# Optimization experiments

Measured on AMD Instinct MI355X. Metric: run time of the kernel, lower is better.

Reference implementation:

```python
import jax, jax.numpy as jnp
import numpy as np
from jax import lax

HEADS = 8
DIM_HEAD = 64
LANDMARKS = 256
PINV_ITERS = 6
KERNEL = 33


def moore_penrose_iter_pinv(x, iters=PINV_ITERS):
    # x: [b, h, m, m]
    abs_x = jnp.abs(x)
    col = abs_x.sum(axis=-1)
    row = abs_x.sum(axis=-2)
    z = jnp.swapaxes(x, -1, -2) / (jnp.max(col) * jnp.max(row) + 1e-12)
    I = jnp.eye(x.shape[-1], dtype=x.dtype)  # broadcasts over b, h
    for _ in range(iters):
        xz = x @ z
        z = 0.25 * z @ (13.0 * I - xz @ (15.0 * I - xz @ (7.0 * I - xz)))
    return z


def setup_inputs() -> dict:
    key = jax.random.key(0)
    k1, k2, k3, k4, k5 = jax.random.split(key, 5)
    b, n, dim = 4, 8192, 512
    inner = HEADS * DIM_HEAD
    x = jax.random.normal(k1, (b, n, dim), dtype=jnp.float32)
    Wqkv = jax.random.normal(k2, (dim, inner * 3), dtype=jnp.float32) * (dim ** -0.5)
    Wout = jax.random.normal(k3, (inner, dim), dtype=jnp.float32) * (inner ** -0.5)
    bout = jax.random.normal(k4, (dim,), dtype=jnp.float32) * 0.02
    conv_w = jax.random.normal(k5, (HEADS, 1, KERNEL, 1), dtype=jnp.float32) * (KERNEL ** -0.5)
    return {"x": x, "Wqkv": Wqkv, "Wout": Wout, "bout": bout, "conv_w": conv_w}


def reference(x, Wqkv, Wout, bout, conv_w):
    b, n, dim = x.shape
    h, d, m = HEADS, DIM_HEAD, LANDMARKS
    scale = d ** -0.5
    # n is a multiple of m, so no left-padding branch; mask is None.
    qkv = x @ Wqkv  # [b, n, 3*h*d]
    q, k, v = jnp.split(qkv, 3, axis=-1)
    tohead = lambda t: t.reshape(b, n, h, d).transpose(0, 2, 1, 3)  # [b,h,n,d]
    q, k, v = tohead(q), tohead(k), tohead(v)
    q = q * scale
    l = n // m  # tokens per landmark group
    qL = q.reshape(b, h, m, l, d).sum(axis=3) / l  # [b,h,m,d]
    kL = k.reshape(b, h, m, l, d).sum(axis=3) / l
    attn1 = jax.nn.softmax(jnp.einsum('bhid,bhjd->bhij', q, kL), axis=-1)   # [b,h,n,m]
    attn2 = jax.nn.softmax(jnp.einsum('bhid,bhjd->bhij', qL, kL), axis=-1)  # [b,h,m,m]
    attn3 = jax.nn.softmax(jnp.einsum('bhid,bhjd->bhij', qL, k), axis=-1)   # [b,h,m,n]
    attn2_pinv = moore_penrose_iter_pinv(attn2, PINV_ITERS)
    out = attn1 @ (attn2_pinv @ (attn3 @ v))  # [b,h,n,d]
    # depthwise residual conv over v viewed as NCHW (C=heads, H=n, W=d)
    pad = KERNEL // 2
    res = lax.conv_general_dilated(
        v, conv_w, window_strides=(1, 1), padding=((pad, pad), (0, 0)),
        dimension_numbers=('NCHW', 'OIHW', 'NCHW'), feature_group_count=h)
    out = out + res
    out = out.transpose(0, 2, 1, 3).reshape(b, n, h * d)
    out = out @ Wout + bout
    return out
```

## Files before the change

kernel.cpp:

```cpp
#include <hip/hip_runtime.h>
#include <hip/hip_bf16.h>
#include <math.h>

#define BB 4
#define NH 8
#define NN 8192
#define DD 64
#define MM 256
#define LG 32
#define DIM 512
#define K3 1536
#define KER 33

typedef __hip_bfloat16 bf16;
typedef __attribute__((ext_vector_type(8))) short bf16x8;
typedef __attribute__((ext_vector_type(4))) float f32x4;

__device__ __forceinline__ float b2f(bf16 x) { return __bfloat162float(x); }
__device__ __forceinline__ bf16 f2b(float x) { return __float2bfloat16(x); }
__device__ __forceinline__ short f2bs(float x) { bf16 h = __float2bfloat16(x); return *reinterpret_cast<short*>(&h); }
__device__ __forceinline__ float bsf(short s) { return __uint_as_float(((unsigned int)(unsigned short)s) << 16); }
__device__ __forceinline__ float blo(unsigned int u) { return __uint_as_float(u << 16); }
__device__ __forceinline__ float bhi(unsigned int u) { return __uint_as_float(u & 0xffff0000u); }

__device__ __forceinline__ void g2lds16(const void* g, void* l) {
    __builtin_amdgcn_global_load_lds(
        (const __attribute__((address_space(1))) unsigned int*)g,
        (__attribute__((address_space(3))) unsigned int*)l, 16, 0, 0);
}

__global__ void zero_out(float* __restrict__ o) {
    o[(size_t)blockIdx.x * 256 + threadIdx.x] = 0.f;
}

__global__ void split_x(const float* __restrict__ x, short* __restrict__ xh,
                        short* __restrict__ xl) {
    size_t i = ((size_t)blockIdx.x * 256 + threadIdx.x) * 8;
    const float4* xp = (const float4*)(x + i);
    float4 v0 = xp[0], v1 = xp[1];
    float vv[8] = {v0.x, v0.y, v0.z, v0.w, v1.x, v1.y, v1.z, v1.w};
    short hb[8], lb[8];
#pragma unroll
    for (int u = 0; u < 8; u++) {
        bf16 h = f2b(vv[u]);
        hb[u] = *(short*)&h;
        lb[u] = f2bs(vv[u] - b2f(h));
    }
    *(uint4*)(xh + i) = *(uint4*)hb;
    *(uint4*)(xl + i) = *(uint4*)lb;
}

__global__ void split_wT(const float* __restrict__ W, short* __restrict__ wh,
                         short* __restrict__ wl, int Nn) {
    int idx = blockIdx.x * 256 + threadIdx.x;
    int k = idx & 511, n = idx >> 9;
    float v = W[(size_t)k * Nn + n];
    bf16 h = f2b(v);
    wh[idx] = *(short*)&h;
    wl[idx] = f2bs(v - b2f(h));
}

__global__ __launch_bounds__(256) void gemm_qkv_mfma(
        const short* __restrict__ xh, const short* __restrict__ xl,
        const short* __restrict__ wh, const short* __restrict__ wl,
        bf16* __restrict__ q, bf16* __restrict__ k, bf16* __restrict__ v) {
    __shared__ short Ah[128 * 32];
    __shared__ short Al[128 * 32];
    __shared__ short Bh[128 * 32];
    __shared__ short Bl[128 * 32];
    int orig = blockIdx.x;
    int wg = (orig & 7) * 384 + (orig >> 3);
    int by = wg / 12, bx = wg - by * 12;
    int rowBase = by * 128, colBase = bx * 128;
    int tid = threadIdx.x;
    int rl = tid >> 2;
    int ch = (tid & 3) * 8;
    int wave = tid >> 6, lane = tid & 63;
    int ln = lane & 15, quad = lane >> 4;
    int wr = (wave >> 1) * 64, wc = (wave & 1) * 64;
    f32x4 acc[4][4];
#pragma unroll
    for (int mt = 0; mt < 4; mt++)
#pragma unroll
        for (int nt = 0; nt < 4; nt++) acc[mt][nt] = (f32x4){0.f, 0.f, 0.f, 0.f};

    for (int k0 = 0; k0 < DIM; k0 += 32) {
        __syncthreads();
#pragma unroll
        for (int p = 0; p < 2; p++) {
            int r = p * 64 + rl;
            size_t ga = (size_t)(rowBase + r) * DIM + k0 + ch;
            size_t gb = (size_t)(colBase + r) * DIM + k0 + ch;
            int lo = r * 32 + ch;
            g2lds16(xh + ga, &Ah[lo]);
            g2lds16(xl + ga, &Al[lo]);
            g2lds16(wh + gb, &Bh[lo]);
            g2lds16(wl + gb, &Bl[lo]);
        }
        __syncthreads();
        bf16x8 a_h[4], a_l[4], b_h[4], b_l[4];
#pragma unroll
        for (int mt = 0; mt < 4; mt++) {
            int o = (wr + mt * 16 + ln) * 32 + quad * 8;
            a_h[mt] = *(const bf16x8*)&Ah[o];
            a_l[mt] = *(const bf16x8*)&Al[o];
        }
#pragma unroll
        for (int nt = 0; nt < 4; nt++) {
            int o = (wc + nt * 16 + ln) * 32 + quad * 8;
            b_h[nt] = *(const bf16x8*)&Bh[o];
            b_l[nt] = *(const bf16x8*)&Bl[o];
        }
#pragma unroll
        for (int mt = 0; mt < 4; mt++)
#pragma unroll
            for (int nt = 0; nt < 4; nt++) {
                acc[mt][nt] = __builtin_amdgcn_mfma_f32_16x16x32_bf16(a_h[mt], b_h[nt], acc[mt][nt], 0, 0, 0);
                acc[mt][nt] = __builtin_amdgcn_mfma_f32_16x16x32_bf16(a_l[mt], b_h[nt], acc[mt][nt], 0, 0, 0);
                acc[mt][nt] = __builtin_amdgcn_mfma_f32_16x16x32_bf16(a_h[mt], b_l[nt], acc[mt][nt], 0, 0, 0);
            }
    }
    int part = colBase >> 9;
    bf16* dst = part == 0 ? q : (part == 1 ? k : v);
    float scale = part == 0 ? 0.125f : 1.0f;
#pragma unroll
    for (int mt = 0; mt < 4; mt++)
#pragma unroll
        for (int nt = 0; nt < 4; nt++)
#pragma unroll
            for (int r = 0; r < 4; r++) {
                int row = rowBase + wr + mt * 16 + quad * 4 + r;
                int col = colBase + wc + nt * 16 + ln;
                int h = (col & 511) >> 6, d = col & 63;
                int b_ = row >> 13, n_ = row & 8191;
                size_t di = ((size_t)(b_ * NH + h) * NN + n_) * DD + d;
                dst[di] = f2b(acc[mt][nt][r] * scale);
            }
}

__global__ __launch_bounds__(256) void gemm_out_mfma(
        const bf16* __restrict__ A, const short* __restrict__ wh,
        const short* __restrict__ wl, const float* __restrict__ bias,
        float* __restrict__ C) {
    __shared__ short As[128 * 32];
    __shared__ short Bh[128 * 32];
    __shared__ short Bl[128 * 32];
    int orig = blockIdx.x;
    int wg = (orig & 7) * 128 + (orig >> 3);
    int by = wg >> 2, bx = wg & 3;
    int rowBase = by * 128, colBase = bx * 128;
    int tid = threadIdx.x;
    int rl = tid >> 2, ch = (tid & 3) * 8;
    int wave = tid >> 6, lane = tid & 63;
    int ln = lane & 15, quad = lane >> 4;
    int wr = (wave >> 1) * 64, wc = (wave & 1) * 64;
    const short* Ab = (const short*)A;
    f32x4 acc[4][4];
#pragma unroll
    for (int mt = 0; mt < 4; mt++)
#pragma unroll
        for (int nt = 0; nt < 4; nt++) acc[mt][nt] = (f32x4){0.f, 0.f, 0.f, 0.f};

    for (int k0 = 0; k0 < DIM; k0 += 32) {
        __syncthreads();
#pragma unroll
        for (int p = 0; p < 2; p++) {
            int r = p * 64 + rl;
            size_t ga = (size_t)(rowBase + r) * DIM + k0 + ch;
            size_t gb = (size_t)(colBase + r) * DIM + k0 + ch;
            int lo = r * 32 + ch;
            g2lds16(Ab + ga, &As[lo]);
            g2lds16(wh + gb, &Bh[lo]);
            g2lds16(wl + gb, &Bl[lo]);
        }
        __syncthreads();
        bf16x8 a[4], b_h[4], b_l[4];
#pragma unroll
        for (int mt = 0; mt < 4; mt++)
            a[mt] = *(const bf16x8*)&As[(wr + mt * 16 + ln) * 32 + quad * 8];
#pragma unroll
        for (int nt = 0; nt < 4; nt++) {
            int o = (wc + nt * 16 + ln) * 32 + quad * 8;
            b_h[nt] = *(const bf16x8*)&Bh[o];
            b_l[nt] = *(const bf16x8*)&Bl[o];
        }
#pragma unroll
        for (int mt = 0; mt < 4; mt++)
#pragma unroll
            for (int nt = 0; nt < 4; nt++) {
                acc[mt][nt] = __builtin_amdgcn_mfma_f32_16x16x32_bf16(a[mt], b_h[nt], acc[mt][nt], 0, 0, 0);
                acc[mt][nt] = __builtin_amdgcn_mfma_f32_16x16x32_bf16(a[mt], b_l[nt], acc[mt][nt], 0, 0, 0);
            }
    }
#pragma unroll
    for (int mt = 0; mt < 4; mt++)
#pragma unroll
        for (int nt = 0; nt < 4; nt++)
#pragma unroll
            for (int r = 0; r < 4; r++) {
                int row = rowBase + wr + mt * 16 + quad * 4 + r;
                int col = colBase + wc + nt * 16 + ln;
                C[(size_t)row * DIM + col] = acc[mt][nt][r] + bias[col];
            }
}

__global__ __launch_bounds__(256) void bgemm_pair(
        const short* __restrict__ Ah, const short* __restrict__ Al,
        const short* __restrict__ Bh, const short* __restrict__ Bl,
        short* __restrict__ oAh, short* __restrict__ oAl,
        short* __restrict__ oBh, short* __restrict__ oBl,
        float* __restrict__ oF, float scale, float alpha, int flags) {
    __shared__ short sAh[64 * 32];
    __shared__ short sAl[64 * 32];
    __shared__ short sBh[64 * 32];
    __shared__ short sBl[64 * 32];
    int bat = blockIdx.z;
    int rowBase = blockIdx.y * 64;
    int colBase = blockIdx.x * 64;
    const size_t MB = (size_t)bat * (MM * MM);
    int tid = threadIdx.x;
    int rl = tid >> 2, ch = (tid & 3) * 8;
    int wave = tid >> 6, lane = tid & 63;
    int ln = lane & 15, quad = lane >> 4;
    int wr = (wave >> 1) * 32, wc = (wave & 1) * 32;
    f32x4 acc[2][2];
#pragma unroll
    for (int mt = 0; mt < 2; mt++)
#pragma unroll
        for (int nt = 0; nt < 2; nt++) acc[mt][nt] = (f32x4){0.f, 0.f, 0.f, 0.f};

    for (int k0 = 0; k0 < MM; k0 += 32) {
        __syncthreads();
        {
            size_t ga = MB + (size_t)(rowBase + rl) * MM + k0 + ch;
            size_t gb = MB + (size_t)(colBase + rl) * MM + k0 + ch;
            int lo = rl * 32 + ch;
            g2lds16(Ah + ga, &sAh[lo]);
            g2lds16(Al + ga, &sAl[lo]);
            g2lds16(Bh + gb, &sBh[lo]);
            g2lds16(Bl + gb, &sBl[lo]);
        }
        __syncthreads();
        bf16x8 a_h[2], a_l[2], b_h[2], b_l[2];
#pragma unroll
        for (int mt = 0; mt < 2; mt++) {
            int o = (wr + mt * 16 + ln) * 32 + quad * 8;
            a_h[mt] = *(const bf16x8*)&sAh[o];
            a_l[mt] = *(const bf16x8*)&sAl[o];
        }
#pragma unroll
        for (int nt = 0; nt < 2; nt++) {
            int o = (wc + nt * 16 + ln) * 32 + quad * 8;
            b_h[nt] = *(const bf16x8*)&sBh[o];
            b_l[nt] = *(const bf16x8*)&sBl[o];
        }
#pragma unroll
        for (int mt = 0; mt < 2; mt++)
#pragma unroll
            for (int nt = 0; nt < 2; nt++) {
                acc[mt][nt] = __builtin_amdgcn_mfma_f32_16x16x32_bf16(a_h[mt], b_h[nt], acc[mt][nt], 0, 0, 0);
                acc[mt][nt] = __builtin_amdgcn_mfma_f32_16x16x32_bf16(a_l[mt], b_h[nt], acc[mt][nt], 0, 0, 0);
                acc[mt][nt] = __builtin_amdgcn_mfma_f32_16x16x32_bf16(a_h[mt], b_l[nt], acc[mt][nt], 0, 0, 0);
            }
    }
#pragma unroll
    for (int mt = 0; mt < 2; mt++)
#pragma unroll
        for (int nt = 0; nt < 2; nt++) {
            short bh4[4], bl4[4];
            int col = colBase + wc + nt * 16 + ln;
            int row0 = rowBase + wr + mt * 16 + quad * 4;
#pragma unroll
            for (int r = 0; r < 4; r++) {
                int row = row0 + r;
                float val = scale * acc[mt][nt][r];
                if (row == col) val += alpha;
                if (flags & 4) oF[MB + (size_t)row * MM + col] = val;
                short vh = f2bs(val);
                short vl = f2bs(val - bsf(vh));
                if (flags & 1) {
                    oAh[MB + (size_t)row * MM + col] = vh;
                    oAl[MB + (size_t)row * MM + col] = vl;
                }
                bh4[r] = vh; bl4[r] = vl;
            }
            if (flags & 2) {
                size_t o = MB + (size_t)col * MM + row0;
                *(uint2*)&oBh[o] = *(uint2*)bh4;
                *(uint2*)&oBl[o] = *(uint2*)bl4;
            }
        }
}

__global__ void eye7_pair(const short* __restrict__ ATh, const short* __restrict__ ATl,
                          short* __restrict__ BTh, short* __restrict__ BTl) {
    size_t base = ((size_t)blockIdx.x * 256 + threadIdx.x) * 8;
    int i0 = (int)(base & 255);
    int j = (int)((base >> 8) & 255);
    uint4 hv = *(const uint4*)&ATh[base];
    uint4 lv = *(const uint4*)&ATl[base];
    unsigned int hu[4] = {hv.x, hv.y, hv.z, hv.w};
    unsigned int lu[4] = {lv.x, lv.y, lv.z, lv.w};
    short ho[8], lo_[8];
#pragma unroll
    for (int u = 0; u < 8; u++) {
        float a = (u & 1 ? bhi(hu[u >> 1]) : blo(hu[u >> 1])) +
                  (u & 1 ? bhi(lu[u >> 1]) : blo(lu[u >> 1]));
        float v = ((i0 + u) == j ? 7.0f : 0.0f) - a;
        short vh = f2bs(v);
        ho[u] = vh;
        lo_[u] = f2bs(v - bsf(vh));
    }
    *(uint4*)&BTh[base] = *(uint4*)ho;
    *(uint4*)&BTl[base] = *(uint4*)lo_;
}

__global__ void z_init_pair(const float* __restrict__ x2, const float* __restrict__ scal,
                            short* __restrict__ zAh, short* __restrict__ zAl,
                            short* __restrict__ zBh, short* __restrict__ zBl) {
    size_t base = ((size_t)blockIdx.x * 256 + threadIdx.x) * 8;
    float inv = 1.0f / (scal[0] * scal[1] + 1e-12f);
    int c0 = (int)(base & 255);
    int r = (int)((base >> 8) & 255);
    size_t MB = (base >> 16) << 16;
    const float4* xp = (const float4*)(x2 + base);
    float4 v0 = xp[0], v1 = xp[1];
    float vv[8] = {v0.x, v0.y, v0.z, v0.w, v1.x, v1.y, v1.z, v1.w};
    short ho[8], lo_[8];
#pragma unroll
    for (int u = 0; u < 8; u++) {
        float v = vv[u] * inv;
        short vh = f2bs(v);
        ho[u] = vh; lo_[u] = f2bs(v - bsf(vh));
    }
    *(uint4*)&zBh[base] = *(uint4*)ho;
    *(uint4*)&zBl[base] = *(uint4*)lo_;
#pragma unroll
    for (int u = 0; u < 8; u++) {
        float v = x2[MB + (size_t)(c0 + u) * MM + r] * inv;
        short vh = f2bs(v);
        ho[u] = vh; lo_[u] = f2bs(v - bsf(vh));
    }
    *(uint4*)&zAh[base] = *(uint4*)ho;
    *(uint4*)&zAl[base] = *(uint4*)lo_;
}

__global__ void bgemm_t2t(const float* __restrict__ A, const float* __restrict__ B,
                          short* __restrict__ T) {
    __shared__ float As[16][64];
    __shared__ float Bs[16][64];
    int bat = blockIdx.z;
    const float* Ab = A + (size_t)bat * MM * MM;
    const float* Bb = B + (size_t)bat * MM * DD;
    short* Tb = T + (size_t)bat * DD * MM;
    int tid = threadIdx.x;
    int rowBase = blockIdx.y * 64;
    int ty = tid >> 4, tx = tid & 15;
    float acc[4][4] = {};
    for (int k0 = 0; k0 < MM; k0 += 16) {
        for (int idx = tid; idx < 64 * 16; idx += 256) {
            int r = idx >> 4, c = idx & 15;
            As[c][r] = Ab[(size_t)(rowBase + r) * MM + k0 + c];
        }
        for (int idx = tid; idx < 16 * 64; idx += 256) {
            int r = idx >> 6, c = idx & 63;
            Bs[r][c] = Bb[(size_t)(k0 + r) * DD + c];
        }
        __syncthreads();
#pragma unroll
        for (int kk = 0; kk < 16; kk++) {
            float a[4], b[4];
#pragma unroll
            for (int i = 0; i < 4; i++) a[i] = As[kk][ty * 4 + i];
#pragma unroll
            for (int j = 0; j < 4; j++) b[j] = Bs[kk][tx * 4 + j];
#pragma unroll
            for (int i = 0; i < 4; i++)
#pragma unroll
                for (int j = 0; j < 4; j++) acc[i][j] += a[i] * b[j];
        }
        __syncthreads();
    }
#pragma unroll
    for (int i = 0; i < 4; i++) {
        int r = rowBase + ty * 4 + i;
#pragma unroll
        for (int j = 0; j < 4; j++) {
            int c = tx * 4 + j;
            Tb[(size_t)c * MM + r] = f2bs(acc[i][j]);
        }
    }
}

__global__ void landmark_means(const bf16* __restrict__ q, const bf16* __restrict__ k,
                               float* __restrict__ qL, float* __restrict__ kL) {
    int idx = blockIdx.x * 256 + threadIdx.x;
    int d = idx & 63;
    int mi = (idx >> 6) & 255;
    int bh = idx >> 14;
    const bf16* qp = q + ((size_t)bh * NN + mi * LG) * DD + d;
    const bf16* kp = k + ((size_t)bh * NN + mi * LG) * DD + d;
    float sq = 0.f, sk = 0.f;
#pragma unroll
    for (int j = 0; j < LG; j++) { sq += b2f(qp[(size_t)j * DD]); sk += b2f(kp[(size_t)j * DD]); }
    qL[idx] = sq * (1.f / LG);
    kL[idx] = sk * (1.f / LG);
}

__global__ void kl_to_bf16(const float* __restrict__ kL, short* __restrict__ kl16) {
    size_t i = ((size_t)blockIdx.x * 256 + threadIdx.x) * 4;
    float4 v = *(const float4*)(kL + i);
    short o[4] = {f2bs(v.x), f2bs(v.y), f2bs(v.z), f2bs(v.w)};
    *(uint2*)&kl16[i] = *(uint2*)o;
}

__global__ void attn2_softmax(const float* __restrict__ qL, const float* __restrict__ kL,
                              float* __restrict__ x2) {
    __shared__ float qs[64];
    __shared__ float red[256];
    int bh = blockIdx.x >> 8, i = blockIdx.x & 255;
    int t = threadIdx.x;
    if (t < 64) qs[t] = qL[((size_t)bh * MM + i) * DD + t];
    __syncthreads();
    const float4* kp = (const float4*)(kL + ((size_t)bh * MM + t) * DD);
    float l = 0.f;
#pragma unroll
    for (int u = 0; u < 16; u++) {
        float4 kv = kp[u];
        l += qs[u*4+0]*kv.x + qs[u*4+1]*kv.y + qs[u*4+2]*kv.z + qs[u*4+3]*kv.w;
    }
    red[t] = l; __syncthreads();
    for (int s = 128; s > 0; s >>= 1) { if (t < s) red[t] = fmaxf(red[t], red[t + s]); __syncthreads(); }
    float mx = red[0]; __syncthreads();
    float e = __expf(l - mx);
    red[t] = e; __syncthreads();
    for (int s = 128; s > 0; s >>= 1) { if (t < s) red[t] += red[t + s]; __syncthreads(); }
    x2[((size_t)bh * MM + i) * MM + t] = e / red[0];
}

__global__ void init_scal(float* scal) {
    if (threadIdx.x == 0) { scal[0] = 0.f; scal[1] = 0.f; }
}

__global__ void rsum_max(const float* __restrict__ x2, float* scal) {
    __shared__ float red[256];
    int t = threadIdx.x;
    float v = fabsf(x2[(size_t)blockIdx.x * MM + t]);
    red[t] = v; __syncthreads();
    for (int s = 128; s > 0; s >>= 1) { if (t < s) red[t] += red[t + s]; __syncthreads(); }
    if (t == 0) atomicMax((unsigned int*)&scal[0], __float_as_uint(red[0]));
}

__global__ void csum_max(const float* __restrict__ x2, float* scal) {
    __shared__ float red[256];
    int t = threadIdx.x;
    const float* xp = x2 + (size_t)blockIdx.x * MM * MM;
    float s = 0.f;
    for (int i = 0; i < MM; i++) s += fabsf(xp[(size_t)i * MM + t]);
    red[t] = s; __syncthreads();
    for (int st = 128; st > 0; st >>= 1) { if (t < st) red[t] = fmaxf(red[t], red[t + st]); __syncthreads(); }
    if (t == 0) atomicMax((unsigned int*)&scal[1], __float_as_uint(red[0]));
}

__global__ void transpose_v(const bf16* __restrict__ v, bf16* __restrict__ vT) {
    int gw = blockIdx.x * 4 + (threadIdx.x >> 6);
    int lane = threadIdx.x & 63;
    int bh = gw >> 8;
    int c  = gw & 255;
    const bf16* vb = v + ((size_t)bh * NN + c * 32) * DD + lane;
    unsigned short buf[32];
#pragma unroll
    for (int i = 0; i < 32; i++) buf[i] = *(const unsigned short*)(vb + (size_t)i * DD);
    bf16* dst = vT + ((size_t)bh * DD + lane) * NN + c * 32;
#pragma unroll
    for (int u = 0; u < 4; u++)
        *(uint4*)(dst + u * 8) = *(uint4*)&buf[u * 8];
}

#define NJ 128
#define KS2 72
#define VS2 136
#define PS2 136
__global__ __launch_bounds__(128, 2) void attn3v_mfma(
        const float* __restrict__ qL, const bf16* __restrict__ k,
        const bf16* __restrict__ vT, float* __restrict__ t1) {
    __shared__ short ks[NJ * KS2];
    __shared__ short vs[DD * VS2];
    __shared__ short ps[2][16 * PS2];
    int g = blockIdx.x;
    int c = g & 7, t = g >> 3;
    int bh = c + 8 * (t >> 3);
    int r0 = (t & 7) * 32;
    int tid = threadIdx.x;
    int wave = tid >> 6, lane = tid & 63;
    int ln = lane & 15, quad = lane >> 4;
    int m = r0 + wave * 16 + ln;
    const float* qrow = qL + ((size_t)bh * MM + m) * DD;
    bf16x8 a0, a1;
#pragma unroll
    for (int u = 0; u < 8; u++) {
        ((short*)&a0)[u] = f2bs(qrow[quad * 8 + u]);
        ((short*)&a1)[u] = f2bs(qrow[32 + quad * 8 + u]);
    }
    const uint4* kg = (const uint4*)(k + (size_t)bh * NN * DD);
    const uint4* vg = (const uint4*)(vT + (size_t)bh * DD * NN);
    float mrow[4], lrow[4];
    f32x4 o[4];
#pragma unroll
    for (int r = 0; r < 4; r++) { mrow[r] = -1e30f; lrow[r] = 0.f; }
#pragma unroll
    for (int ct = 0; ct < 4; ct++) o[ct] = (f32x4){0.f, 0.f, 0.f, 0.f};
    short* pw = &ps[wave][0];

    for (int j0 = 0; j0 < NN; j0 += NJ) {
        __syncthreads();
#pragma unroll
        for (int it = 0; it < 8; it++) {
            int idx = it * 128 + tid;
            int row = idx >> 3, c8 = idx & 7;
            uint4 pk = kg[(size_t)(j0 + row) * 8 + c8];
            *(uint4*)&ks[row * KS2 + c8 * 8] = pk;
        }
#pragma unroll
        for (int it = 0; it < 8; it++) {
            int idx = it * 128 + tid;
            int row = idx >> 4, c8 = idx & 15;
            uint4 pv = vg[(size_t)row * (NN / 8) + (j0 / 8) + c8];
            *(uint4*)&vs[row * VS2 + c8 * 8] = pv;
        }
        __syncthreads();
        f32x4 s[8];
#pragma unroll
        for (int ct = 0; ct < 8; ct++) {
            const short* kp = &ks[(ct * 16 + ln) * KS2 + quad * 8];
            bf16x8 b0 = *(const bf16x8*)kp;
            bf16x8 b1 = *(const bf16x8*)(kp + 32);
            f32x4 cc = {0.f, 0.f, 0.f, 0.f};
            cc = __builtin_amdgcn_mfma_f32_16x16x32_bf16(a0, b0, cc, 0, 0, 0);
            cc = __builtin_amdgcn_mfma_f32_16x16x32_bf16(a1, b1, cc, 0, 0, 0);
            s[ct] = cc;
        }
#pragma unroll
        for (int r = 0; r < 4; r++) {
            float v = -1e30f;
#pragma unroll
            for (int ct = 0; ct < 8; ct++) v = fmaxf(v, s[ct][r]);
            v = fmaxf(v, __shfl_xor(v, 1));
            v = fmaxf(v, __shfl_xor(v, 2));
            v = fmaxf(v, __shfl_xor(v, 4));
            v = fmaxf(v, __shfl_xor(v, 8));
            float mn = fmaxf(mrow[r], v);
            float alpha = __expf(mrow[r] - mn);
            mrow[r] = mn;
            float psum = 0.f;
#pragma unroll
            for (int ct = 0; ct < 8; ct++) { float e = __expf(s[ct][r] - mn); s[ct][r] = e; psum += e; }
            lrow[r] = lrow[r] * alpha + psum;
#pragma unroll
            for (int c2 = 0; c2 < 4; c2++) o[c2][r] *= alpha;
        }
#pragma unroll
        for (int ct = 0; ct < 8; ct++)
#pragma unroll
            for (int r = 0; r < 4; r++)
                pw[(quad * 4 + r) * PS2 + ct * 16 + ln] = f2bs(s[ct][r]);
#pragma unroll
        for (int kstep = 0; kstep < 4; kstep++) {
            bf16x8 pa = *(const bf16x8*)&pw[ln * PS2 + kstep * 32 + quad * 8];
#pragma unroll
            for (int ct = 0; ct < 4; ct++) {
                bf16x8 pb = *(const bf16x8*)&vs[(ct * 16 + ln) * VS2 + kstep * 32 + quad * 8];
                o[ct] = __builtin_amdgcn_mfma_f32_16x16x32_bf16(pa, pb, o[ct], 0, 0, 0);
            }
        }
    }
#pragma unroll
    for (int r = 0; r < 4; r++) {
        float l = lrow[r];
        l += __shfl_xor(l, 1);
        l += __shfl_xor(l, 2);
        l += __shfl_xor(l, 4);
        l += __shfl_xor(l, 8);
        lrow[r] = 1.0f / l;
    }
#pragma unroll
    for (int ct = 0; ct < 4; ct++)
#pragma unroll
        for (int r = 0; r < 4; r++) {
            int row = r0 + wave * 16 + quad * 4 + r;
            t1[((size_t)bh * MM + row) * DD + ct * 16 + ln] = o[ct][r] * lrow[r];
        }
}

#define KLS 72
#define T2S 264
__global__ __launch_bounds__(256, 1) void attn1_mfma(
        const bf16* __restrict__ q, const short* __restrict__ kl16,
        const short* __restrict__ t2t, bf16* __restrict__ oh) {
    __shared__ short kls[MM * KLS];
    __shared__ short t2s[DD * T2S];
    __shared__ short ps1[4][16 * T2S];
    int bh = blockIdx.y;
    int n0 = blockIdx.x * 64;
    int tid = threadIdx.x;
    const short* kLb = kl16 + (size_t)bh * MM * DD;
    for (int idx = tid; idx < MM * DD / 8; idx += 256) {
        int l = idx >> 3, d8 = (idx & 7) * 8;
        *(uint4*)&kls[l * KLS + d8] = *(const uint4*)&kLb[idx * 8];
    }
    const short* t2b = t2t + (size_t)bh * DD * MM;
    for (int idx = tid; idx < DD * MM / 8; idx += 256) {
        int c = idx >> 5, r = (idx & 31) * 8;
        *(uint4*)&t2s[c * T2S + r] = *(const uint4*)&t2b[idx * 8];
    }
    __syncthreads();
    int wave = tid >> 6, lane = tid & 63;
    int ln = lane & 15, quad = lane >> 4;
    int m = n0 + wave * 16 + ln;
    const bf16* qrow = q + ((size_t)bh * NN + m) * DD;
    bf16x8 a0 = *(const bf16x8*)(qrow + quad * 8);
    bf16x8 a1 = *(const bf16x8*)(qrow + 32 + quad * 8);
    f32x4 acc[16];
#pragma unroll
    for (int nt = 0; nt < 16; nt++) {
        const short* kp = &kls[(nt * 16 + ln) * KLS + quad * 8];
        bf16x8 b0 = *(const bf16x8*)kp;
        bf16x8 b1 = *(const bf16x8*)(kp + 32);
        f32x4 c = {0.f, 0.f, 0.f, 0.f};
        c = __builtin_amdgcn_mfma_f32_16x16x32_bf16(a0, b0, c, 0, 0, 0);
        c = __builtin_amdgcn_mfma_f32_16x16x32_bf16(a1, b1, c, 0, 0, 0);
        acc[nt] = c;
    }
    float inv[4];
#pragma unroll
    for (int r = 0; r < 4; r++) {
        float v = -1e30f;
#pragma unroll
        for (int nt = 0; nt < 16; nt++) v = fmaxf(v, acc[nt][r]);
        v = fmaxf(v, __shfl_xor(v, 1));
        v = fmaxf(v, __shfl_xor(v, 2));
        v = fmaxf(v, __shfl_xor(v, 4));
        v = fmaxf(v, __shfl_xor(v, 8));
        float s = 0.f;
#pragma unroll
        for (int nt = 0; nt < 16; nt++) { float e = __expf(acc[nt][r] - v); acc[nt][r] = e; s += e; }
        s += __shfl_xor(s, 1);
        s += __shfl_xor(s, 2);
        s += __shfl_xor(s, 4);
        s += __shfl_xor(s, 8);
        inv[r] = 1.0f / s;
    }
    short* pw = &ps1[wave][0];
#pragma unroll
    for (int nt = 0; nt < 16; nt++)
#pragma unroll
        for (int r = 0; r < 4; r++)
            pw[(quad * 4 + r) * T2S + nt * 16 + ln] = f2bs(acc[nt][r]);
    __syncthreads();
    f32x4 o[4];
#pragma unroll
    for (int nt = 0; nt < 4; nt++) o[nt] = (f32x4){0.f, 0.f, 0.f, 0.f};
#pragma unroll
    for (int ks = 0; ks < 8; ks++) {
        bf16x8 pa = *(const bf16x8*)&pw[ln * T2S + ks * 32 + quad * 8];
#pragma unroll
        for (int nt = 0; nt < 4; nt++) {
            bf16x8 pb = *(const bf16x8*)&t2s[(nt * 16 + ln) * T2S + ks * 32 + quad * 8];
            o[nt] = __builtin_amdgcn_mfma_f32_16x16x32_bf16(pa, pb, o[nt], 0, 0, 0);
        }
    }
    int b_ = bh >> 3, h = bh & 7;
#pragma unroll
    for (int nt = 0; nt < 4; nt++)
#pragma unroll
        for (int r = 0; r < 4; r++) {
            int row = n0 + wave * 16 + quad * 4 + r;
            int col = nt * 16 + ln;
            oh[((size_t)(b_ * NN + row)) * DIM + h * 64 + col] = f2b(o[nt][r] * inv[r]);
        }
}

__global__ __launch_bounds__(256) void conv_add2(const bf16* __restrict__ v,
                                                 const float* __restrict__ w,
                                                 bf16* __restrict__ oh) {
    int tid = threadIdx.x;
    int c = tid & 7;
    int nsub = tid >> 3;
    int bh = blockIdx.x >> 8;
    int n = ((blockIdx.x & 255) << 5) + nsub;
    int b_ = bh >> 3, h = bh & 7;
    const bf16* vb = v + (size_t)bh * NN * DD + c * 8;
    float acc[8] = {};
#pragma unroll
    for (int t = 0; t < KER; t++) {
        int src = n + t - 16;
        if (src >= 0 && src < NN) {
            uint4 pk = *(const uint4*)(vb + (size_t)src * DD);
            float wt = w[h * KER + t];
            unsigned int ua[4] = {pk.x, pk.y, pk.z, pk.w};
#pragma unroll
            for (int j = 0; j < 4; j++) {
                acc[2 * j]     += wt * blo(ua[j]);
                acc[2 * j + 1] += wt * bhi(ua[j]);
            }
        }
    }
    size_t oidx = ((size_t)(b_ * NN + n)) * DIM + h * 64 + c * 8;
    uint4 cur = *(uint4*)&oh[oidx];
    unsigned int cu[4] = {cur.x, cur.y, cur.z, cur.w};
    short outp[8];
#pragma unroll
    for (int j = 0; j < 4; j++) {
        outp[2 * j]     = f2bs(blo(cu[j]) + acc[2 * j]);
        outp[2 * j + 1] = f2bs(bhi(cu[j]) + acc[2 * j + 1]);
    }
    *(uint4*)&oh[oidx] = *(uint4*)outp;
}


extern "C" void kernel_launch(void* const* d_in, const int* in_sizes, int n_in,
                              void* d_out, int out_size, void* d_ws, size_t ws_size,
                              hipStream_t stream) {
    const float* x    = (const float*)d_in[0];
    const float* Wqkv = (const float*)d_in[1];
    const float* Wout = (const float*)d_in[2];
    const float* bout = (const float*)d_in[3];
    const float* cw   = (const float*)d_in[4];
    float* out = (float*)d_out;

    const size_t SZ_QKV = (size_t)BB * NH * NN * DD;
    const size_t SZ_L   = (size_t)BB * NH * MM * DD;
    const size_t SZ_M2  = (size_t)BB * NH * MM * MM;

    char* p = (char*)d_ws;
    bf16* q    = (bf16*)p;  p += SZ_QKV * 2;
    bf16* v    = (bf16*)p;  p += SZ_QKV * 2;
    float* x2   = (float*)p; p += SZ_M2 * 4;
    float* zf   = (float*)p; p += SZ_M2 * 4;
    float* z2r  = (float*)p; p += SZ_M2 * 4;
    float* bAr  = (float*)p; p += SZ_M2 * 4;
    float* bBr  = (float*)p; p += SZ_M2 * 4;
    float* qL   = (float*)p; p += SZ_L * 4;
    float* kL   = (float*)p; p += SZ_L * 4;
    float* t1   = (float*)p; p += SZ_L * 4;
    short* t2t  = (short*)p; p += SZ_L * 4;
    float* scal = (float*)p; p += 2 * 4;
    size_t need = (size_t)(p - (char*)d_ws);
    bf16* k  = (bf16*)d_out;
    bf16* vT = (bf16*)d_out + SZ_QKV;
    bf16* oh = (bf16*)x2;

    short* xh  = (short*)x2;
    short* xl  = (short*)vT;
    short* wqh = (short*)bBr;
    short* wql = (short*)bBr + (size_t)K3 * DIM;
    short* woh = (short*)q;
    short* wol = (short*)q + (size_t)DIM * DIM;
    short* kl16 = (short*)t1;

    const size_t U = SZ_M2;
    short* db = (short*)d_out;
    short* bufBTh = db + 0 * U;  short* bufBTl = db + 1 * U;
    short* z2BTh  = db + 2 * U;  short* z2BTl  = db + 3 * U;
    short* zPair[2][4] = {
        { db + 4 * U, db + 5 * U, db + 6 * U, db + 7 * U },
        { db + 8 * U, db + 9 * U, db + 10 * U, db + 11 * U } };
    short* x2Ah = (short*)z2r;   short* x2Al = (short*)z2r + U;
    short* bufAh = (short*)bAr;  short* bufAl = (short*)bAr + U;
    short* bufATh = (short*)bBr; short* bufATl = (short*)bBr + U;

    if (ws_size < need) {
        zero_out<<<out_size / 256, 256, 0, stream>>>(out);
        return;
    }

    split_x<<<(int)(SZ_QKV / (256 * 8)), 256, 0, stream>>>(x, xh, xl);
    split_wT<<<(K3 * DIM) / 256, 256, 0, stream>>>(Wqkv, wqh, wql, K3);
    gemm_qkv_mfma<<<3072, 256, 0, stream>>>(xh, xl, wqh, wql, q, k, v);
    transpose_v<<<(BB * NH * MM) / 4, 256, 0, stream>>>(v, vT);
    landmark_means<<<(BB * NH * MM * DD) / 256, 256, 0, stream>>>(q, k, qL, kL);
    attn2_softmax<<<BB * NH * MM, 256, 0, stream>>>(qL, kL, x2);
    attn3v_mfma<<<256, 128, 0, stream>>>(qL, k, vT, t1);
    init_scal<<<1, 64, 0, stream>>>(scal);
    rsum_max<<<BB * NH * MM, 256, 0, stream>>>(x2, scal);
    csum_max<<<BB * NH, 256, 0, stream>>>(x2, scal);
    z_init_pair<<<(int)(SZ_M2 / (256 * 8)), 256, 0, stream>>>(
        x2, scal, zPair[0][0], zPair[0][1], zPair[0][2], zPair[0][3]);
    split_x<<<(int)(SZ_M2 / (256 * 8)), 256, 0, stream>>>(x2, x2Ah, x2Al);
    int cur = 0;
    for (int it = 0; it < 6; it++) {
        int nxt = cur ^ 1;
        bgemm_pair<<<dim3(4, 4, BB * NH), 256, 0, stream>>>(
            x2Ah, x2Al, zPair[cur][2], zPair[cur][3],
            bufAh, bufAl, bufATh, bufATl, nullptr, 1.f, 0.f, 1 | 2);
        eye7_pair<<<(int)(SZ_M2 / (256 * 8)), 256, 0, stream>>>(
            bufATh, bufATl, bufBTh, bufBTl);
        bgemm_pair<<<dim3(4, 4, BB * NH), 256, 0, stream>>>(
            bufAh, bufAl, bufBTh, bufBTl,
            nullptr, nullptr, z2BTh, z2BTl, nullptr, -1.f, 15.f, 2);
        bgemm_pair<<<dim3(4, 4, BB * NH), 256, 0, stream>>>(
            bufAh, bufAl, z2BTh, z2BTl,
            nullptr, nullptr, bufBTh, bufBTl, nullptr, -1.f, 13.f, 2);
        int fl = (it == 5) ? 4 : (1 | 2);
        bgemm_pair<<<dim3(4, 4, BB * NH), 256, 0, stream>>>(
            zPair[cur][0], zPair[cur][1], bufBTh, bufBTl,
            zPair[nxt][0], zPair[nxt][1], zPair[nxt][2], zPair[nxt][3],
            zf, 0.25f, 0.f, fl);
        cur = nxt;
    }
    bgemm_t2t<<<dim3(1, 4, BB * NH), 256, 0, stream>>>(zf, t1, t2t);
    kl_to_bf16<<<(int)(SZ_L / (256 * 4)), 256, 0, stream>>>(kL, kl16);
    attn1_mfma<<<dim3(NN / 64, BB * NH), 256, 0, stream>>>(q, kl16, t2t, oh);
    conv_add2<<<BB * NH * 256, 256, 0, stream>>>(v, cw, oh);
    split_wT<<<(DIM * DIM) / 256, 256, 0, stream>>>(Wout, woh, wol, DIM);
    gemm_out_mfma<<<1024, 256, 0, stream>>>(oh, woh, wol, bout, out);

    (void)in_sizes; (void)n_in; (void)ws_size;
}
```

Measured before the change: 1.181 ms.

## Fuse conv residual into attn1, identity update into GEMM epilogue, drop row-sum pass

The depthwise residual conv now runs inside the attn1 kernel, from a haloed V tile staged in LDS, and is added before the single store to oh. This removes the separate conv_add2 read-modify-write of oh and its repeated V reads. The 7I - XZ step of the pinv iteration moves into the bgemm_pair epilogue through new scaleB/alphaB parameters, which removes the eye7_pair kernel from each of the six iterations. z_init and the x2 hi/lo split become one kernel. The rsum_max reduction is dropped, relying on softmax rows of attn2 summing to one. This adds LDS use and register pressure in attn1, and the normaliser now depends on the softmax row-sum property.

```diff
diff --git a/kernel.cpp b/kernel.cpp
--- a/kernel.cpp
+++ b/kernel.cpp
@@ -209,7 +209,8 @@
         const short* __restrict__ Bh, const short* __restrict__ Bl,
         short* __restrict__ oAh, short* __restrict__ oAl,
         short* __restrict__ oBh, short* __restrict__ oBl,
-        float* __restrict__ oF, float scale, float alpha, int flags) {
+        float* __restrict__ oF, float scale, float alpha,
+        float scaleB, float alphaB, int flags) {
     __shared__ short sAh[64 * 32];
     __shared__ short sAl[64 * 32];
     __shared__ short sBh[64 * 32];
@@ -276,13 +277,15 @@
                 float val = scale * acc[mt][nt][r];
                 if (row == col) val += alpha;
                 if (flags & 4) oF[MB + (size_t)row * MM + col] = val;
-                short vh = f2bs(val);
-                short vl = f2bs(val - bsf(vh));
                 if (flags & 1) {
+                    short vh = f2bs(val);
                     oAh[MB + (size_t)row * MM + col] = vh;
-                    oAl[MB + (size_t)row * MM + col] = vl;
+                    oAl[MB + (size_t)row * MM + col] = f2bs(val - bsf(vh));
                 }
-                bh4[r] = vh; bl4[r] = vl;
+                float bv = scaleB * val;
+                if (row == col) bv += alphaB;
+                short bvh = f2bs(bv);
+                bh4[r] = bvh; bl4[r] = f2bs(bv - bsf(bvh));
             }
             if (flags & 2) {
                 size_t o = MB + (size_t)col * MM + row0;
@@ -292,47 +295,29 @@
         }
 }
 
-__global__ void eye7_pair(const short* __restrict__ ATh, const short* __restrict__ ATl,
-                          short* __restrict__ BTh, short* __restrict__ BTl) {
+__global__ void z_init_split(const float* __restrict__ x2, const float* __restrict__ scal,
+                             short* __restrict__ x2Ah, short* __restrict__ x2Al,
+                             short* __restrict__ zAh, short* __restrict__ zAl,
+                             short* __restrict__ zBh, short* __restrict__ zBl) {
     size_t base = ((size_t)blockIdx.x * 256 + threadIdx.x) * 8;
-    int i0 = (int)(base & 255);
-    int j = (int)((base >> 8) & 255);
-    uint4 hv = *(const uint4*)&ATh[base];
-    uint4 lv = *(const uint4*)&ATl[base];
-    unsigned int hu[4] = {hv.x, hv.y, hv.z, hv.w};
-    unsigned int lu[4] = {lv.x, lv.y, lv.z, lv.w};
-    short ho[8], lo_[8];
-#pragma unroll
-    for (int u = 0; u < 8; u++) {
-        float a = (u & 1 ? bhi(hu[u >> 1]) : blo(hu[u >> 1])) +
-                  (u & 1 ? bhi(lu[u >> 1]) : blo(lu[u >> 1]));
-        float v = ((i0 + u) == j ? 7.0f : 0.0f) - a;
-        short vh = f2bs(v);
-        ho[u] = vh;
-        lo_[u] = f2bs(v - bsf(vh));
-    }
-    *(uint4*)&BTh[base] = *(uint4*)ho;
-    *(uint4*)&BTl[base] = *(uint4*)lo_;
-}
-
-__global__ void z_init_pair(const float* __restrict__ x2, const float* __restrict__ scal,
-                            short* __restrict__ zAh, short* __restrict__ zAl,
-                            short* __restrict__ zBh, short* __restrict__ zBl) {
-    size_t base = ((size_t)blockIdx.x * 256 + threadIdx.x) * 8;
-    float inv = 1.0f / (scal[0] * scal[1] + 1e-12f);
+    float inv = 1.0f / (scal[0] + 1e-12f);
     int c0 = (int)(base & 255);
     int r = (int)((base >> 8) & 255);
     size_t MB = (base >> 16) << 16;
     const float4* xp = (const float4*)(x2 + base);
     float4 v0 = xp[0], v1 = xp[1];
     float vv[8] = {v0.x, v0.y, v0.z, v0.w, v1.x, v1.y, v1.z, v1.w};
-    short ho[8], lo_[8];
+    short ho[8], lo_[8], h2[8], l2[8];
 #pragma unroll
     for (int u = 0; u < 8; u++) {
-        float v = vv[u] * inv;
-        short vh = f2bs(v);
-        ho[u] = vh; lo_[u] = f2bs(v - bsf(vh));
-    }
+        short xh = f2bs(vv[u]);
+        h2[u] = xh; l2[u] = f2bs(vv[u] - bsf(xh));
+        float zv = vv[u] * inv;
+        short zh = f2bs(zv);
+        ho[u] = zh; lo_[u] = f2bs(zv - bsf(zh));
+    }
+    *(uint4*)&x2Ah[base] = *(uint4*)h2;
+    *(uint4*)&x2Al[base] = *(uint4*)l2;
     *(uint4*)&zBh[base] = *(uint4*)ho;
     *(uint4*)&zBl[base] = *(uint4*)lo_;
 #pragma unroll
@@ -442,15 +427,6 @@
     if (threadIdx.x == 0) { scal[0] = 0.f; scal[1] = 0.f; }
 }
 
-__global__ void rsum_max(const float* __restrict__ x2, float* scal) {
-    __shared__ float red[256];
-    int t = threadIdx.x;
-    float v = fabsf(x2[(size_t)blockIdx.x * MM + t]);
-    red[t] = v; __syncthreads();
-    for (int s = 128; s > 0; s >>= 1) { if (t < s) red[t] += red[t + s]; __syncthreads(); }
-    if (t == 0) atomicMax((unsigned int*)&scal[0], __float_as_uint(red[0]));
-}
-
 __global__ void csum_max(const float* __restrict__ x2, float* scal) {
     __shared__ float red[256];
     int t = threadIdx.x;
@@ -459,7 +435,7 @@
     for (int i = 0; i < MM; i++) s += fabsf(xp[(size_t)i * MM + t]);
     red[t] = s; __syncthreads();
     for (int st = 128; st > 0; st >>= 1) { if (t < st) red[t] = fmaxf(red[t], red[t + st]); __syncthreads(); }
-    if (t == 0) atomicMax((unsigned int*)&scal[1], __float_as_uint(red[0]));
+    if (t == 0) atomicMax((unsigned int*)&scal[0], __float_as_uint(red[0]));
 }
 
 __global__ void transpose_v(const bf16* __restrict__ v, bf16* __restrict__ vT) {
@@ -594,15 +570,19 @@
 
 #define KLS 72
 #define T2S 264
+#define VLS 72
 __global__ __launch_bounds__(256, 1) void attn1_mfma(
         const bf16* __restrict__ q, const short* __restrict__ kl16,
-        const short* __restrict__ t2t, bf16* __restrict__ oh) {
+        const short* __restrict__ t2t, const bf16* __restrict__ v,
+        const float* __restrict__ cw, bf16* __restrict__ oh) {
     __shared__ short kls[MM * KLS];
     __shared__ short t2s[DD * T2S];
     __shared__ short ps1[4][16 * T2S];
+    __shared__ short vload[96 * VLS];
     int bh = blockIdx.y;
     int n0 = blockIdx.x * 64;
     int tid = threadIdx.x;
+    int b_ = bh >> 3, h = bh & 7;
     const short* kLb = kl16 + (size_t)bh * MM * DD;
     for (int idx = tid; idx < MM * DD / 8; idx += 256) {
         int l = idx >> 3, d8 = (idx & 7) * 8;
@@ -612,6 +592,15 @@
     for (int idx = tid; idx < DD * MM / 8; idx += 256) {
         int c = idx >> 5, r = (idx & 31) * 8;
         *(uint4*)&t2s[c * T2S + r] = *(const uint4*)&t2b[idx * 8];
+    }
+    const bf16* vb = v + (size_t)bh * NN * DD;
+    for (int idx = tid; idx < 96 * 8; idx += 256) {
+        int row = idx >> 3, c8 = (idx & 7) * 8;
+        int gn = n0 - 16 + row;
+        uint4 pv;
+        pv.x = pv.y = pv.z = pv.w = 0u;
+        if (gn >= 0 && gn < NN) pv = *(const uint4*)(vb + (size_t)gn * DD + c8);
+        *(uint4*)&vload[row * VLS + c8] = pv;
     }
     __syncthreads();
     int wave = tid >> 6, lane = tid & 63;
@@ -634,16 +623,16 @@
     float inv[4];
 #pragma unroll
     for (int r = 0; r < 4; r++) {
-        float v = -1e30f;
-#pragma unroll
-        for (int nt = 0; nt < 16; nt++) v = fmaxf(v, acc[nt][r]);
-        v = fmaxf(v, __shfl_xor(v, 1));
-        v = fmaxf(v, __shfl_xor(v, 2));
-        v = fmaxf(v, __shfl_xor(v, 4));
-        v = fmaxf(v, __shfl_xor(v, 8));
+        float vx = -1e30f;
+#pragma unroll
+        for (int nt = 0; nt < 16; nt++) vx = fmaxf(vx, acc[nt][r]);
+        vx = fmaxf(vx, __shfl_xor(vx, 1));
+        vx = fmaxf(vx, __shfl_xor(vx, 2));
+        vx = fmaxf(vx, __shfl_xor(vx, 4));
+        vx = fmaxf(vx, __shfl_xor(vx, 8));
         float s = 0.f;
 #pragma unroll
-        for (int nt = 0; nt < 16; nt++) { float e = __expf(acc[nt][r] - v); acc[nt][r] = e; s += e; }
+        for (int nt = 0; nt < 16; nt++) { float e = __expf(acc[nt][r] - vx); acc[nt][r] = e; s += e; }
         s += __shfl_xor(s, 1);
         s += __shfl_xor(s, 2);
         s += __shfl_xor(s, 4);
@@ -669,52 +658,28 @@
             o[nt] = __builtin_amdgcn_mfma_f32_16x16x32_bf16(pa, pb, o[nt], 0, 0, 0);
         }
     }
-    int b_ = bh >> 3, h = bh & 7;
-#pragma unroll
-    for (int nt = 0; nt < 4; nt++)
+    const float* wrow = cw + h * KER;
+    int lbase = wave * 16 + quad * 4;
+#pragma unroll
+    for (int nt = 0; nt < 4; nt++) {
+        int d = nt * 16 + ln;
+        float win[36];
+#pragma unroll
+        for (int j = 0; j < 36; j++)
+            win[j] = bsf(vload[(lbase + j) * VLS + d]);
+        float res[4] = {0.f, 0.f, 0.f, 0.f};
+#pragma unroll
+        for (int t = 0; t < KER; t++) {
+            float wt = wrow[t];
+#pragma unroll
+            for (int r = 0; r < 4; r++) res[r] += wt * win[r + t];
+        }
 #pragma unroll
         for (int r = 0; r < 4; r++) {
-            int row = n0 + wave * 16 + quad * 4 + r;
-            int col = nt * 16 + ln;
-            oh[((size_t)(b_ * NN + row)) * DIM + h * 64 + col] = f2b(o[nt][r] * inv[r]);
-        }
-}
-
-__global__ __launch_bounds__(256) void conv_add2(const bf16* __restrict__ v,
-                                                 const float* __restrict__ w,
-                                                 bf16* __restrict__ oh) {
-    int tid = threadIdx.x;
-    int c = tid & 7;
-    int nsub = tid >> 3;
-    int bh = blockIdx.x >> 8;
-    int n = ((blockIdx.x & 255) << 5) + nsub;
-    int b_ = bh >> 3, h = bh & 7;
-    const bf16* vb = v + (size_t)bh * NN * DD + c * 8;
-    float acc[8] = {};
-#pragma unroll
-    for (int t = 0; t < KER; t++) {
-        int src = n + t - 16;
-        if (src >= 0 && src < NN) {
-            uint4 pk = *(const uint4*)(vb + (size_t)src * DD);
-            float wt = w[h * KER + t];
-            unsigned int ua[4] = {pk.x, pk.y, pk.z, pk.w};
-#pragma unroll
-            for (int j = 0; j < 4; j++) {
-                acc[2 * j]     += wt * blo(ua[j]);
-                acc[2 * j + 1] += wt * bhi(ua[j]);
-            }
-        }
-    }
-    size_t oidx = ((size_t)(b_ * NN + n)) * DIM + h * 64 + c * 8;
-    uint4 cur = *(uint4*)&oh[oidx];
-    unsigned int cu[4] = {cur.x, cur.y, cur.z, cur.w};
-    short outp[8];
-#pragma unroll
-    for (int j = 0; j < 4; j++) {
-        outp[2 * j]     = f2bs(blo(cu[j]) + acc[2 * j]);
-        outp[2 * j + 1] = f2bs(bhi(cu[j]) + acc[2 * j + 1]);
-    }
-    *(uint4*)&oh[oidx] = *(uint4*)outp;
+            int row = n0 + lbase + r;
+            oh[((size_t)(b_ * NN + row)) * DIM + h * 64 + d] = f2b(o[nt][r] * inv[r] + res[r]);
+        }
+    }
 }
 
 
@@ -767,7 +732,6 @@
         { db + 8 * U, db + 9 * U, db + 10 * U, db + 11 * U } };
     short* x2Ah = (short*)z2r;   short* x2Al = (short*)z2r + U;
     short* bufAh = (short*)bAr;  short* bufAl = (short*)bAr + U;
-    short* bufATh = (short*)bBr; short* bufATl = (short*)bBr + U;
 
     if (ws_size < need) {
         zero_out<<<out_size / 256, 256, 0, stream>>>(out);
@@ -782,36 +746,35 @@
     attn2_softmax<<<BB * NH * MM, 256, 0, stream>>>(qL, kL, x2);
     attn3v_mfma<<<256, 128, 0, stream>>>(qL, k, vT, t1);
     init_scal<<<1, 64, 0, stream>>>(scal);
-    rsum_max<<<BB * NH * MM, 256, 0, stream>>>(x2, scal);
     csum_max<<<BB * NH, 256, 0, stream>>>(x2, scal);
-    z_init_pair<<<(int)(SZ_M2 / (256 * 8)), 256, 0, stream>>>(
-        x2, scal, zPair[0][0], zPair[0][1], zPair[0][2], zPair[0][3]);
-    split_x<<<(int)(SZ_M2 / (256 * 8)), 256, 0, stream>>>(x2, x2Ah, x2Al);
+    z_init_split<<<(int)(SZ_M2 / (256 * 8)), 256, 0, stream>>>(
+        x2, scal, x2Ah, x2Al,
+        zPair[0][0], zPair[0][1], zPair[0][2], zPair[0][3]);
     int cur = 0;
     for (int it = 0; it < 6; it++) {
         int nxt = cur ^ 1;
         bgemm_pair<<<dim3(4, 4, BB * NH), 256, 0, stream>>>(
             x2Ah, x2Al, zPair[cur][2], zPair[cur][3],
-            bufAh, bufAl, bufATh, bufATl, nullptr, 1.f, 0.f, 1 | 2);
-        eye7_pair<<<(int)(SZ_M2 / (256 * 8)), 256, 0, stream>>>(
-            bufATh, bufATl, bufBTh, bufBTl);
+            bufAh, bufAl, bufBTh, bufBTl, nullptr,
+            1.f, 0.f, -1.f, 7.f, 1 | 2);
         bgemm_pair<<<dim3(4, 4, BB * NH), 256, 0, stream>>>(
             bufAh, bufAl, bufBTh, bufBTl,
-            nullptr, nullptr, z2BTh, z2BTl, nullptr, -1.f, 15.f, 2);
+            nullptr, nullptr, z2BTh, z2BTl, nullptr,
+            -1.f, 15.f, 1.f, 0.f, 2);
         bgemm_pair<<<dim3(4, 4, BB * NH), 256, 0, stream>>>(
             bufAh, bufAl, z2BTh, z2BTl,
-            nullptr, nullptr, bufBTh, bufBTl, nullptr, -1.f, 13.f, 2);
+            nullptr, nullptr, bufBTh, bufBTl, nullptr,
+            -1.f, 13.f, 1.f, 0.f, 2);
         int fl = (it == 5) ? 4 : (1 | 2);
         bgemm_pair<<<dim3(4, 4, BB * NH), 256, 0, stream>>>(
             zPair[cur][0], zPair[cur][1], bufBTh, bufBTl,
             zPair[nxt][0], zPair[nxt][1], zPair[nxt][2], zPair[nxt][3],
-            zf, 0.25f, 0.f, fl);
+            zf, 0.25f, 0.f, 1.f, 0.f, fl);
         cur = nxt;
     }
     bgemm_t2t<<<dim3(1, 4, BB * NH), 256, 0, stream>>>(zf, t1, t2t);
     kl_to_bf16<<<(int)(SZ_L / (256 * 4)), 256, 0, stream>>>(kL, kl16);
-    attn1_mfma<<<dim3(NN / 64, BB * NH), 256, 0, stream>>>(q, kl16, t2t, oh);
-    conv_add2<<<BB * NH * 256, 256, 0, stream>>>(v, cw, oh);
+    attn1_mfma<<<dim3(NN / 64, BB * NH), 256, 0, stream>>>(q, kl16, t2t, v, cw, oh);
     split_wT<<<(DIM * DIM) / 256, 256, 0, stream>>>(Wout, woh, wol, DIM);
     gemm_out_mfma<<<1024, 256, 0, stream>>>(oh, woh, wol, bout, out);
 
```

Measured after the change: 1.062 ms. -10.1%, faster.
